# Performance work log

Hardware: AMD Instinct MI355X
Metric: run time of the kernel (lower is better)

## Reference

```python
import jax, jax.numpy as jnp
import numpy as np

B, L, ENC, EMB, H, V = 64, 33, 512, 256, 512, 32000


def setup_inputs() -> dict:
    key = jax.random.key(0)
    ks = jax.random.split(key, 16)
    x = jax.random.normal(ks[0], (B, ENC), dtype=jnp.float32)
    padded_target = jax.random.randint(ks[1], (B, L), 0, V)
    target_lengths = jax.random.randint(ks[2], (B,), 2, L + 1)
    target_lengths = target_lengths.at[0].set(L)  # pin max length -> static step count
    s = 0.05
    return {
        "x": x,
        "padded_target": padded_target,
        "target_lengths": target_lengths,
        "embed": jax.random.normal(ks[3], (V, EMB), dtype=jnp.float32) * s,
        "W_h0": jax.random.normal(ks[4], (H, ENC), dtype=jnp.float32) * s,
        "b_h0": jnp.zeros((H,), jnp.float32),
        "W_c0": jax.random.normal(ks[5], (H, ENC), dtype=jnp.float32) * s,
        "b_c0": jnp.zeros((H,), jnp.float32),
        "W_ih": jax.random.normal(ks[6], (4 * H, ENC + EMB), dtype=jnp.float32) * s,
        "W_hh": jax.random.normal(ks[7], (4 * H, H), dtype=jnp.float32) * s,
        "b_ih": jnp.zeros((4 * H,), jnp.float32),
        "b_hh": jnp.zeros((4 * H,), jnp.float32),
        "W_out": jax.random.normal(ks[8], (V, H), dtype=jnp.float32) * s,
        "b_out": jnp.zeros((V,), jnp.float32),
    }


def reference(x, padded_target, target_lengths, embed, W_h0, b_h0, W_c0, b_c0,
              W_ih, W_hh, b_ih, b_hh, W_out, b_out):
    # sort by length, descending (packed-sequence ordering)
    sorted_indices = jnp.argsort(-target_lengths)
    x = x[sorted_indices]                      # [B, ENC]
    tgt = padded_target[sorted_indices]        # [B, L]
    lens = target_lengths[sorted_indices] - 1  # decode steps per row
    emb = embed[tgt]                           # [B, L, EMB]

    h = x @ W_h0.T + b_h0                      # context-initialized state
    c = x @ W_c0.T + b_c0
    T = padded_target.shape[1] - 1             # static max steps (max len pinned to L)

    def step(carry, inp):
        h, c = carry
        e_t, t = inp
        active = (lens > t)[:, None]           # rows still decoding (prefix, sorted)
        g = jnp.concatenate([x, e_t], axis=1) @ W_ih.T + b_ih + h @ W_hh.T + b_hh
        i, f, gg, o = jnp.split(g, 4, axis=1)  # torch LSTMCell gate order i,f,g,o
        c_new = jax.nn.sigmoid(f) * c + jax.nn.sigmoid(i) * jnp.tanh(gg)
        h_new = jax.nn.sigmoid(o) * jnp.tanh(c_new)
        h = jnp.where(active, h_new, h)        # inactive rows keep frozen state
        c = jnp.where(active, c_new, c)
        pred = jnp.where(active, h_new @ W_out.T + b_out, 0.0)  # dropout p=0
        return (h, c), pred

    (_, _), preds = jax.lax.scan(
        step, (h, c), (jnp.transpose(emb[:, :T], (1, 0, 2)), jnp.arange(T)))
    prediction = jnp.transpose(preds, (1, 0, 2))  # [B, T, V]
    return prediction, sorted_indices
```

## Files before the change

### kernel.cpp

```cpp
#include <hip/hip_runtime.h>

typedef __attribute__((ext_vector_type(8))) short short8;
typedef __attribute__((ext_vector_type(8))) unsigned short ushort8;
typedef __attribute__((ext_vector_type(4))) float f32x4;

#define DEV __device__ __forceinline__

DEV unsigned short f2bf(float f) {
  unsigned int u = __float_as_uint(f);
  u += 0x7fffu + ((u >> 16) & 1u);
  return (unsigned short)(u >> 16);
}
DEV float sigm(float x) { return 1.f / (1.f + __expf(-x)); }
DEV float tanh_(float x) { return 1.f - 2.f / (1.f + __expf(2.f * x)); }

typedef __attribute__((address_space(1))) const void* as1cv;
typedef __attribute__((address_space(3))) void* as3v;
DEV void gll16(const void* g, void* l) {
  __builtin_amdgcn_global_load_lds((as1cv)g, (as3v)l, 16, 0, 0);
}

__global__ void __launch_bounds__(256) k_pre(const float* __restrict__ x,
    const int* __restrict__ ptar, const int* __restrict__ tlen,
    const float* __restrict__ W_h0, const float* __restrict__ W_c0,
    const float* __restrict__ W_ih, const float* __restrict__ W_hh,
    int* __restrict__ sidx, int* __restrict__ lens, int* __restrict__ base,
    int* __restrict__ inv, int* __restrict__ Pw, int* __restrict__ tok,
    unsigned short* __restrict__ xsb, float* __restrict__ tail,
    unsigned short* __restrict__ Wpro, unsigned short* __restrict__ Wihb2,
    unsigned short* __restrict__ Whb) {
  int bid = blockIdx.x, tid = threadIdx.x;
  if (bid > 0) {
    long long g = (long long)(bid - 1) * 2048 + tid * 8;
    const float* src;
    unsigned short* dst;
    if (g < 262144) {
      src = W_h0 + g; dst = Wpro + g;
    } else if (g < 524288) {
      long long l = g - 262144; src = W_c0 + l; dst = Wpro + 262144 + l;
    } else if (g < 1572864) {
      long long l = g - 524288;
      long long r = l >> 9, c = l & 511;
      src = W_ih + r * 768 + c; dst = Wpro + 524288 + l;
    } else if (g < 2097152) {
      long long l = g - 1572864;
      long long r = l >> 8, c = l & 255;
      src = W_ih + r * 768 + 512 + c; dst = Wihb2 + l;
    } else {
      long long l = g - 2097152; src = W_hh + l; dst = Whb + l;
    }
    float4 v0 = *(const float4*)src, v1 = *(const float4*)(src + 4);
    ushort8 o;
    o[0] = f2bf(v0.x); o[1] = f2bf(v0.y); o[2] = f2bf(v0.z); o[3] = f2bf(v0.w);
    o[4] = f2bf(v1.x); o[5] = f2bf(v1.y); o[6] = f2bf(v1.z); o[7] = f2bf(v1.w);
    *(ushort8*)dst = o;
    return;
  }
  __shared__ int ss[64], ls[64], bs[64];
  if (tid < 64) {
    int li = tlen[tid];
    int rank = 0;
    for (int j = 0; j < 64; ++j) {
      int lj = tlen[j];
      rank += (lj > li || (lj == li && j < tid)) ? 1 : 0;
    }
    ss[rank] = tid;
  }
  __syncthreads();
  if (tid < 64) {
    int src = ss[tid];
    sidx[tid] = src;
    int l = tlen[src] - 1;
    ls[tid] = l;
    lens[tid] = l;
    tail[tid] = (float)src;
  }
  __syncthreads();
  if (tid == 0) {
    int s = 0;
    for (int b = 0; b < 64; ++b) { bs[b] = s; base[b] = s; s += ls[b]; }
    Pw[0] = s;
  }
  __syncthreads();
  for (int idx = tid; idx < 2048; idx += 256) {
    int b = idx >> 5, t = idx & 31;
    if (t < ls[b]) inv[bs[b] + t] = idx;
  }
  for (int idx = tid; idx < 32 * 64; idx += 256) {
    int t = idx >> 6, b = idx & 63;
    tok[idx] = ptar[ss[b] * 33 + t];
  }
  for (int idx = tid; idx < 64 * 512; idx += 256) {
    int b = idx >> 9;
    xsb[idx] = f2bf(x[ss[b] * 512 + (idx & 511)]);
  }
}

__global__ void __launch_bounds__(256) k_mid(const unsigned short* __restrict__ xsb,
    const unsigned short* __restrict__ Wpro, const float* __restrict__ b_h0,
    const float* __restrict__ b_c0, const float* __restrict__ b_ih,
    const float* __restrict__ b_hh, unsigned short* __restrict__ h0b,
    float* __restrict__ c, float* __restrict__ gx,
    const int* __restrict__ tok, const float* __restrict__ embed,
    unsigned short* __restrict__ Eb) {
  int bid = blockIdx.x, tid = threadIdx.x;
  if (bid >= 48) {
    int gid = (bid - 48) * 256 + tid;
    int row = gid >> 5, c8 = (gid & 31) * 8;
    const float* src = embed + (size_t)tok[row] * 256 + c8;
    float4 v0 = *(const float4*)src, v1 = *(const float4*)(src + 4);
    ushort8 o;
    o[0] = f2bf(v0.x); o[1] = f2bf(v0.y); o[2] = f2bf(v0.z); o[3] = f2bf(v0.w);
    o[4] = f2bf(v1.x); o[5] = f2bf(v1.y); o[6] = f2bf(v1.z); o[7] = f2bf(v1.w);
    *(ushort8*)(Eb + (size_t)row * 256 + c8) = o;
    return;
  }
  int lane = tid & 63, w = tid >> 6;
  int n0 = bid * 64 + w * 16;
  int lr = lane & 15, lk = lane >> 4;
  f32x4 acc[4];
#pragma unroll
  for (int i = 0; i < 4; ++i) acc[i] = (f32x4){0.f, 0.f, 0.f, 0.f};
  const unsigned short* B = Wpro + (size_t)(n0 + lr) * 512 + lk * 8;
  const unsigned short* A = xsb + (size_t)lr * 512 + lk * 8;
#pragma unroll
  for (int ks = 0; ks < 16; ++ks) {
    short8 bfr = *(const short8*)(B + ks * 32);
#pragma unroll
    for (int mi = 0; mi < 4; ++mi) {
      short8 af = *(const short8*)(A + mi * 16 * 512 + ks * 32);
      acc[mi] = __builtin_amdgcn_mfma_f32_16x16x32_bf16(af, bfr, acc[mi], 0, 0, 0);
    }
  }
  int n = n0 + lr;
#pragma unroll
  for (int mi = 0; mi < 4; ++mi)
#pragma unroll
    for (int r = 0; r < 4; ++r) {
      int b = mi * 16 + lk * 4 + r;
      float v = acc[mi][r];
      if (n < 512) {
        h0b[b * 512 + n] = f2bf(v + b_h0[n]);
      } else if (n < 1024) {
        int u = n - 512;
        c[b * 512 + u] = v + b_c0[u];
      } else {
        int j = n - 1024;
        gx[(size_t)b * 2048 + j] = v + b_ih[j] + b_hh[j];
      }
    }
}

__global__ void __launch_bounds__(256) k_ga2(const unsigned short* __restrict__ Eb,
    const unsigned short* __restrict__ Wb2, const float* __restrict__ gx,
    float* __restrict__ GA) {
  __shared__ alignas(16) char ldsbuf[32768];
  char* ldsA = ldsbuf;
  char* ldsB = ldsbuf + 16384;
  int bid = blockIdx.x, tid = threadIdx.x;
  int mt = bid & 15, nt = bid >> 4;
  int m0 = mt * 128, n0 = nt * 128;
  int lane = tid & 63, w = tid >> 6;
  int wm = w >> 1, wn = w & 1;
  f32x4 acc[4][4];
#pragma unroll
  for (int a = 0; a < 4; ++a)
#pragma unroll
    for (int bq = 0; bq < 4; ++bq) acc[a][bq] = (f32x4){0.f, 0.f, 0.f, 0.f};
  const unsigned short* Arow = Eb + (size_t)m0 * 256;
  const unsigned short* Brow = Wb2 + (size_t)n0 * 256;
  for (int kt = 0; kt < 4; ++kt) {
    int k0 = kt * 64;
    if (kt) __syncthreads();
#pragma unroll
    for (int j = 0; j < 4; ++j) {
      int ci = j * 256 + w * 64 + lane;
      int r = ci >> 3;
      int clog = ((ci & 7) << 4) ^ ((r & 7) << 4);
      int ldst = (j * 256 + w * 64) * 16;
      gll16((const char*)(Arow + (size_t)r * 256 + k0) + clog, ldsA + ldst);
      gll16((const char*)(Brow + (size_t)r * 256 + k0) + clog, ldsB + ldst);
    }
    __syncthreads();
#pragma unroll
    for (int kk = 0; kk < 2; ++kk) {
      short8 af[4], bf[4];
      int cb = kk * 64 + (lane >> 4) * 16;
#pragma unroll
      for (int i = 0; i < 4; ++i) {
        int ar = wm * 64 + i * 16 + (lane & 15);
        af[i] = *(const short8*)(ldsA + ar * 128 + (cb ^ ((ar & 7) << 4)));
        int br = wn * 64 + i * 16 + (lane & 15);
        bf[i] = *(const short8*)(ldsB + br * 128 + (cb ^ ((br & 7) << 4)));
      }
#pragma unroll
      for (int mi = 0; mi < 4; ++mi)
#pragma unroll
        for (int ni = 0; ni < 4; ++ni)
          acc[mi][ni] = __builtin_amdgcn_mfma_f32_16x16x32_bf16(
              af[mi], bf[ni], acc[mi][ni], 0, 0, 0);
    }
  }
#pragma unroll
  for (int mi = 0; mi < 4; ++mi) {
    int mb = m0 + wm * 64 + mi * 16 + ((lane >> 4) << 2);
#pragma unroll
    for (int r = 0; r < 4; ++r) {
      int m = mb + r;
#pragma unroll
      for (int ni = 0; ni < 4; ++ni) {
        int j = n0 + wn * 64 + ni * 16 + (lane & 15);
        GA[(size_t)m * 2048 + j] = acc[mi][ni][r] + gx[(size_t)(m & 63) * 2048 + j];
      }
    }
  }
}

__global__ void __launch_bounds__(256) k_step4(
    const unsigned short* __restrict__ hin, unsigned short* __restrict__ hout,
    float* __restrict__ c, const float* __restrict__ GA,
    const unsigned short* __restrict__ Whb, const int* __restrict__ lens,
    const int* __restrict__ base, unsigned short* __restrict__ Hm,
    const float* __restrict__ W_out, unsigned short* __restrict__ Wob, int t) {
  int tid = threadIdx.x, bid = blockIdx.x;
  if (bid >= 128) {
    long long s0 = (long long)t * 512000 + (long long)(bid - 128) * 8000;
    long long s1 = s0 + 8000;
    for (long long i = s0 + tid * 8; i < s1; i += 2048) {
      float4 v0 = *(const float4*)(W_out + i);
      float4 v1 = *(const float4*)(W_out + i + 4);
      ushort8 o;
      o[0] = f2bf(v0.x); o[1] = f2bf(v0.y); o[2] = f2bf(v0.z); o[3] = f2bf(v0.w);
      o[4] = f2bf(v1.x); o[5] = f2bf(v1.y); o[6] = f2bf(v1.z); o[7] = f2bf(v1.w);
      *(ushort8*)(Wob + i) = o;
    }
    return;
  }
  int lane = tid & 63, w = tid >> 6;
  int lr = lane & 15, lk = lane >> 4;
  int mq = bid & 3, ug = bid >> 2;
  int r0 = mq * 16;
  int gate = lr >> 2, ul = lr & 3;
  int u = ug * 16 + w * 4 + ul;

  const float* gab = GA + ((size_t)t * 64 + r0) * 2048 + gate * 512 + u;
  float gv[4];
#pragma unroll
  for (int r = 0; r < 4; ++r) gv[r] = gab[(size_t)(lk * 4 + r) * 2048];

  const unsigned short* Bp = Whb + ((size_t)gate * 512 + u) * 512 + lk * 8;
  const unsigned short* Ap = hin + (size_t)(r0 + lr) * 512 + lk * 8;
  f32x4 acc = (f32x4){0.f, 0.f, 0.f, 0.f};
#pragma unroll
  for (int ks = 0; ks < 16; ++ks) {
    short8 a0 = *(const short8*)(Ap + ks * 32);
    short8 b0 = *(const short8*)(Bp + ks * 32);
    acc = __builtin_amdgcn_mfma_f32_16x16x32_bf16(a0, b0, acc, 0, 0, 0);
  }
#pragma unroll
  for (int r = 0; r < 4; ++r) {
    float v = acc[r] + gv[r];
    float av = (gate == 2) ? tanh_(v) : sigm(v);
    float x4 = __shfl_xor(av, 4);
    float x8 = __shfl_xor(av, 8);
    float x12 = __shfl_xor(av, 12);
    float vi = (gate == 0) ? av : (gate == 1) ? x4 : (gate == 2) ? x8 : x12;
    float vf = (gate == 1) ? av : (gate == 0) ? x4 : (gate == 3) ? x8 : x12;
    float vg = (gate == 2) ? av : (gate == 3) ? x4 : (gate == 0) ? x8 : x12;
    float vo = (gate == 3) ? av : (gate == 2) ? x4 : (gate == 1) ? x8 : x12;
    if (gate == 0) {
      int b = r0 + lk * 4 + r;
      float cold = c[b * 512 + u];
      float cn = vf * cold + vi * vg;
      float hn = vo * tanh_(cn);
      bool act = lens[b] > t;
      if (act) c[b * 512 + u] = cn;
      unsigned short hbv = f2bf(hn);
      hout[b * 512 + u] = act ? hbv : hin[b * 512 + u];
      if (act) Hm[((size_t)(base[b] + t)) * 512 + u] = hbv;
    }
  }
}

__global__ void __launch_bounds__(256) k_gemm(const unsigned short* __restrict__ Hm,
    const unsigned short* __restrict__ Wb, const float* __restrict__ b_out,
    const int* __restrict__ inv, const int* __restrict__ Pw,
    const int* __restrict__ lens, float* __restrict__ out) {
  int bid = blockIdx.x, tid = threadIdx.x;
  if (bid >= 4000) {
    int idx = bid - 4000;
    float4 z = {0.f, 0.f, 0.f, 0.f};
#pragma unroll
    for (int k = 0; k < 4; ++k) {
      int m = idx * 4 + k;
      int b = m >> 5, t = m & 31;
      if (lens[b] > t) continue;
      float* row = out + (size_t)m * 32000;
      for (int i = tid * 4; i < 32000; i += 1024) *(float4*)(row + i) = z;
    }
    return;
  }
  __shared__ alignas(16) char ldsbuf[32768];
  char* ldsA = ldsbuf;
  char* ldsB = ldsbuf + 16384;
  int P = Pw[0];
  int sb = (bid & 7) * 500 + (bid >> 3);
  int mt = sb & 15, nt = sb >> 4;
  int m0 = mt * 128, n0 = nt * 128;
  if (m0 >= P) return;
  int lane = tid & 63, w = tid >> 6;
  int wm = w >> 1, wn = w & 1;
  f32x4 acc[4][4];
#pragma unroll
  for (int a = 0; a < 4; ++a)
#pragma unroll
    for (int bq = 0; bq < 4; ++bq) acc[a][bq] = (f32x4){0.f, 0.f, 0.f, 0.f};
  const unsigned short* Arow = Hm + (size_t)m0 * 512;
  const unsigned short* Brow = Wb + (size_t)n0 * 512;
  for (int kt = 0; kt < 8; ++kt) {
    int k0 = kt * 64;
    if (kt) __syncthreads();
#pragma unroll
    for (int j = 0; j < 4; ++j) {
      int ci = j * 256 + w * 64 + lane;
      int r = ci >> 3;
      int clog = ((ci & 7) << 4) ^ ((r & 7) << 4);
      int ldst = (j * 256 + w * 64) * 16;
      gll16((const char*)(Arow + (size_t)r * 512 + k0) + clog, ldsA + ldst);
      gll16((const char*)(Brow + (size_t)r * 512 + k0) + clog, ldsB + ldst);
    }
    __syncthreads();
#pragma unroll
    for (int kk = 0; kk < 2; ++kk) {
      short8 af[4], bf[4];
      int cb = kk * 64 + (lane >> 4) * 16;
#pragma unroll
      for (int i = 0; i < 4; ++i) {
        int ar = wm * 64 + i * 16 + (lane & 15);
        af[i] = *(const short8*)(ldsA + ar * 128 + (cb ^ ((ar & 7) << 4)));
        int br = wn * 64 + i * 16 + (lane & 15);
        bf[i] = *(const short8*)(ldsB + br * 128 + (cb ^ ((br & 7) << 4)));
      }
#pragma unroll
      for (int mi = 0; mi < 4; ++mi)
#pragma unroll
        for (int ni = 0; ni < 4; ++ni)
          acc[mi][ni] = __builtin_amdgcn_mfma_f32_16x16x32_bf16(
              af[mi], bf[ni], acc[mi][ni], 0, 0, 0);
    }
  }
#pragma unroll
  for (int mi = 0; mi < 4; ++mi) {
    int pb = m0 + wm * 64 + mi * 16 + ((lane >> 4) << 2);
#pragma unroll
    for (int r = 0; r < 4; ++r) {
      int p = pb + r;
      if (p >= P) continue;
      size_t orow = (size_t)inv[p] * 32000;
#pragma unroll
      for (int ni = 0; ni < 4; ++ni) {
        int n = n0 + wn * 64 + ni * 16 + (lane & 15);
        out[orow + n] = acc[mi][ni][r] + b_out[n];
      }
    }
  }
}

extern "C" void kernel_launch(void* const* d_in, const int* in_sizes, int n_in,
                              void* d_out, int out_size, void* d_ws, size_t ws_size,
                              hipStream_t stream) {
  const float* x     = (const float*)d_in[0];
  const int*   ptar  = (const int*)d_in[1];
  const int*   tlen  = (const int*)d_in[2];
  const float* embed = (const float*)d_in[3];
  const float* W_h0  = (const float*)d_in[4];
  const float* b_h0  = (const float*)d_in[5];
  const float* W_c0  = (const float*)d_in[6];
  const float* b_c0  = (const float*)d_in[7];
  const float* W_ih  = (const float*)d_in[8];
  const float* W_hh  = (const float*)d_in[9];
  const float* b_ih  = (const float*)d_in[10];
  const float* b_hh  = (const float*)d_in[11];
  const float* W_out = (const float*)d_in[12];
  const float* b_out = (const float*)d_in[13];
  float* out = (float*)d_out;

  char* ws = (char*)d_ws;
  size_t off = 0;
  auto alloc = [&](size_t bytes) {
    void* p = ws + off;
    off += (bytes + 255) & ~(size_t)255;
    return p;
  };
  unsigned short* Wob = (unsigned short*)alloc(32000ull * 512 * 2);
  unsigned short* Hm  = (unsigned short*)alloc(2048ull * 512 * 2);
  unsigned short* h0b = (unsigned short*)alloc(64 * 512 * 2);
  unsigned short* h1b = (unsigned short*)alloc(64 * 512 * 2);
  float* cbuf = (float*)alloc(64 * 512 * 4);
  float* gx   = (float*)alloc(64 * 2048 * 4);
  int* sidx = (int*)alloc(64 * 4);
  int* lens = (int*)alloc(64 * 4);
  int* base = (int*)alloc(64 * 4);
  int* inv  = (int*)alloc(2048 * 4);
  int* Pw   = (int*)alloc(4);
  int* tok  = (int*)alloc(2048 * 4);

  float* GA = out;
  unsigned short* Wpro  = (unsigned short*)(out + 4194304);
  unsigned short* Wihb2 = (unsigned short*)(out + 4980736);
  unsigned short* Whb   = (unsigned short*)(out + 5242880);
  unsigned short* Eb    = (unsigned short*)(out + 5767168);
  unsigned short* xsb   = (unsigned short*)(out + 6029312);
  float* tail = out + 65536000;

  k_pre<<<1537, 256, 0, stream>>>(x, ptar, tlen, W_h0, W_c0, W_ih, W_hh,
                                  sidx, lens, base, inv, Pw, tok, xsb, tail,
                                  Wpro, Wihb2, Whb);
  k_mid<<<304, 256, 0, stream>>>(xsb, Wpro, b_h0, b_c0, b_ih, b_hh, h0b, cbuf,
                                 gx, tok, embed, Eb);
  k_ga2<<<256, 256, 0, stream>>>(Eb, Wihb2, gx, GA);

  unsigned short* hb[2] = {h0b, h1b};
  for (int t = 0; t < 32; ++t)
    k_step4<<<192, 256, 0, stream>>>(hb[t & 1], hb[(t + 1) & 1], cbuf, GA, Whb,
                                     lens, base, Hm, W_out, Wob, t);

  k_gemm<<<4512, 256, 0, stream>>>(Hm, Wob, b_out, inv, Pw, lens, out);
  (void)in_sizes; (void)n_in; (void)out_size; (void)ws_size;
}
```

Before: 394.4 us.

## Move W_out bf16 conversion into k_ga2 and load GEMM A operand directly

The fp32-to-bf16 conversion of W_out, previously spread across the 32 recurrent step launches as extra blocks, now runs as 500 extra blocks of the one-shot k_ga2 launch. This makes each step kernel smaller and possibly lowers per-step latency. In the output GEMM, the A operand (hidden states) is now read straight from global memory into registers instead of being staged through LDS, which halves the shared memory per block. The trade-off is uncoalesced, unswizzled global reads for A, which may rely on cache hits.

Result: slower. 450.7 us (+14.3%).

```diff
diff --git a/kernel.cpp b/kernel.cpp
--- a/kernel.cpp
+++ b/kernel.cpp
@@ -153,11 +153,26 @@
 
 __global__ void __launch_bounds__(256) k_ga2(const unsigned short* __restrict__ Eb,
     const unsigned short* __restrict__ Wb2, const float* __restrict__ gx,
-    float* __restrict__ GA) {
+    float* __restrict__ GA, const float* __restrict__ W_out,
+    unsigned short* __restrict__ Wob) {
+  int bid = blockIdx.x, tid = threadIdx.x;
+  if (bid >= 256) {
+    long long basei = (long long)(bid - 256) * 32768;
+#pragma unroll 4
+    for (int it = 0; it < 16; ++it) {
+      long long i = basei + (long long)it * 2048 + tid * 8;
+      float4 v0 = *(const float4*)(W_out + i);
+      float4 v1 = *(const float4*)(W_out + i + 4);
+      ushort8 o;
+      o[0] = f2bf(v0.x); o[1] = f2bf(v0.y); o[2] = f2bf(v0.z); o[3] = f2bf(v0.w);
+      o[4] = f2bf(v1.x); o[5] = f2bf(v1.y); o[6] = f2bf(v1.z); o[7] = f2bf(v1.w);
+      *(ushort8*)(Wob + i) = o;
+    }
+    return;
+  }
   __shared__ alignas(16) char ldsbuf[32768];
   char* ldsA = ldsbuf;
   char* ldsB = ldsbuf + 16384;
-  int bid = blockIdx.x, tid = threadIdx.x;
   int mt = bid & 15, nt = bid >> 4;
   int m0 = mt * 128, n0 = nt * 128;
   int lane = tid & 63, w = tid >> 6;
@@ -220,22 +235,8 @@
     const unsigned short* __restrict__ hin, unsigned short* __restrict__ hout,
     float* __restrict__ c, const float* __restrict__ GA,
     const unsigned short* __restrict__ Whb, const int* __restrict__ lens,
-    const int* __restrict__ base, unsigned short* __restrict__ Hm,
-    const float* __restrict__ W_out, unsigned short* __restrict__ Wob, int t) {
+    const int* __restrict__ base, unsigned short* __restrict__ Hm, int t) {
   int tid = threadIdx.x, bid = blockIdx.x;
-  if (bid >= 128) {
-    long long s0 = (long long)t * 512000 + (long long)(bid - 128) * 8000;
-    long long s1 = s0 + 8000;
-    for (long long i = s0 + tid * 8; i < s1; i += 2048) {
-      float4 v0 = *(const float4*)(W_out + i);
-      float4 v1 = *(const float4*)(W_out + i + 4);
-      ushort8 o;
-      o[0] = f2bf(v0.x); o[1] = f2bf(v0.y); o[2] = f2bf(v0.z); o[3] = f2bf(v0.w);
-      o[4] = f2bf(v1.x); o[5] = f2bf(v1.y); o[6] = f2bf(v1.z); o[7] = f2bf(v1.w);
-      *(ushort8*)(Wob + i) = o;
-    }
-    return;
-  }
   int lane = tid & 63, w = tid >> 6;
   int lr = lane & 15, lk = lane >> 4;
   int mq = bid & 3, ug = bid >> 2;
@@ -300,9 +301,7 @@
     }
     return;
   }
-  __shared__ alignas(16) char ldsbuf[32768];
-  char* ldsA = ldsbuf;
-  char* ldsB = ldsbuf + 16384;
+  __shared__ alignas(16) char ldsB[16384];
   int P = Pw[0];
   int sb = (bid & 7) * 500 + (bid >> 3);
   int mt = sb & 15, nt = sb >> 4;
@@ -315,7 +314,7 @@
   for (int a = 0; a < 4; ++a)
 #pragma unroll
     for (int bq = 0; bq < 4; ++bq) acc[a][bq] = (f32x4){0.f, 0.f, 0.f, 0.f};
-  const unsigned short* Arow = Hm + (size_t)m0 * 512;
+  const char* Ab = (const char*)(Hm + (size_t)m0 * 512);
   const unsigned short* Brow = Wb + (size_t)n0 * 512;
   for (int kt = 0; kt < 8; ++kt) {
     int k0 = kt * 64;
@@ -325,19 +324,25 @@
       int ci = j * 256 + w * 64 + lane;
       int r = ci >> 3;
       int clog = ((ci & 7) << 4) ^ ((r & 7) << 4);
-      int ldst = (j * 256 + w * 64) * 16;
-      gll16((const char*)(Arow + (size_t)r * 512 + k0) + clog, ldsA + ldst);
-      gll16((const char*)(Brow + (size_t)r * 512 + k0) + clog, ldsB + ldst);
-    }
-    __syncthreads();
-#pragma unroll
-    for (int kk = 0; kk < 2; ++kk) {
-      short8 af[4], bf[4];
-      int cb = kk * 64 + (lane >> 4) * 16;
+      gll16((const char*)(Brow + (size_t)r * 512 + k0) + clog,
+            ldsB + (j * 256 + w * 64) * 16);
+    }
+    short8 af2[2][4];
+#pragma unroll
+    for (int kk = 0; kk < 2; ++kk)
 #pragma unroll
       for (int i = 0; i < 4; ++i) {
         int ar = wm * 64 + i * 16 + (lane & 15);
-        af[i] = *(const short8*)(ldsA + ar * 128 + (cb ^ ((ar & 7) << 4)));
+        int cb = kk * 64 + (lane >> 4) * 16;
+        af2[kk][i] = *(const short8*)(Ab + (size_t)ar * 1024 + k0 * 2 + cb);
+      }
+    __syncthreads();
+#pragma unroll
+    for (int kk = 0; kk < 2; ++kk) {
+      short8 bf[4];
+      int cb = kk * 64 + (lane >> 4) * 16;
+#pragma unroll
+      for (int i = 0; i < 4; ++i) {
         int br = wn * 64 + i * 16 + (lane & 15);
         bf[i] = *(const short8*)(ldsB + br * 128 + (cb ^ ((br & 7) << 4)));
       }
@@ -346,7 +351,7 @@
 #pragma unroll
         for (int ni = 0; ni < 4; ++ni)
           acc[mi][ni] = __builtin_amdgcn_mfma_f32_16x16x32_bf16(
-              af[mi], bf[ni], acc[mi][ni], 0, 0, 0);
+              af2[kk][mi], bf[ni], acc[mi][ni], 0, 0, 0);
     }
   }
 #pragma unroll
@@ -418,12 +423,12 @@
                                   Wpro, Wihb2, Whb);
   k_mid<<<304, 256, 0, stream>>>(xsb, Wpro, b_h0, b_c0, b_ih, b_hh, h0b, cbuf,
                                  gx, tok, embed, Eb);
-  k_ga2<<<256, 256, 0, stream>>>(Eb, Wihb2, gx, GA);
+  k_ga2<<<756, 256, 0, stream>>>(Eb, Wihb2, gx, GA, W_out, Wob);
 
   unsigned short* hb[2] = {h0b, h1b};
   for (int t = 0; t < 32; ++t)
-    k_step4<<<192, 256, 0, stream>>>(hb[t & 1], hb[(t + 1) & 1], cbuf, GA, Whb,
-                                     lens, base, Hm, W_out, Wob, t);
+    k_step4<<<128, 256, 0, stream>>>(hb[t & 1], hb[(t + 1) & 1], cbuf, GA, Whb,
+                                     lens, base, Hm, t);
 
   k_gemm<<<4512, 256, 0, stream>>>(Hm, Wob, b_out, inv, Pw, lens, out);
   (void)in_sizes; (void)n_in; (void)out_size; (void)ws_size;
```

## Fuse 32 LSTM step launches into one persistent kernel with grid barrier

Applied to the files above, without the earlier changes.

Replaces the per-timestep launches of the recurrent step kernel with a single persistent kernel. Its 128 compute blocks loop over the timesteps and synchronise through atomic counters in global memory, which k_pre zeroes. Blocks whose row-group has finished decoding skip the step compute but still join each barrier. The W_out to bf16 conversion now runs in 128 extra blocks that stream through the whole weight at once instead of one slice per step. This removes launch overhead, but it depends on all 256 blocks being co-resident and adds spin-wait latency on every step.

After: 653.8 us. +65.8%, slower.

```diff
diff --git a/kernel.cpp b/kernel.cpp
--- a/kernel.cpp
+++ b/kernel.cpp
@@ -28,7 +28,7 @@
     int* __restrict__ inv, int* __restrict__ Pw, int* __restrict__ tok,
     unsigned short* __restrict__ xsb, float* __restrict__ tail,
     unsigned short* __restrict__ Wpro, unsigned short* __restrict__ Wihb2,
-    unsigned short* __restrict__ Whb) {
+    unsigned short* __restrict__ Whb, int* __restrict__ bar) {
   int bid = blockIdx.x, tid = threadIdx.x;
   if (bid > 0) {
     long long g = (long long)(bid - 1) * 2048 + tid * 8;
@@ -57,6 +57,7 @@
     return;
   }
   __shared__ int ss[64], ls[64], bs[64];
+  if (tid < 32) bar[tid] = 0;
   if (tid < 64) {
     int li = tlen[tid];
     int rank = 0;
@@ -216,17 +217,17 @@
   }
 }
 
-__global__ void __launch_bounds__(256) k_step4(
-    const unsigned short* __restrict__ hin, unsigned short* __restrict__ hout,
+__global__ void __launch_bounds__(256) k_steps_p(
+    unsigned short* __restrict__ h0, unsigned short* __restrict__ h1,
     float* __restrict__ c, const float* __restrict__ GA,
     const unsigned short* __restrict__ Whb, const int* __restrict__ lens,
     const int* __restrict__ base, unsigned short* __restrict__ Hm,
-    const float* __restrict__ W_out, unsigned short* __restrict__ Wob, int t) {
+    int* __restrict__ bar,
+    const float* __restrict__ W_out, unsigned short* __restrict__ Wob) {
   int tid = threadIdx.x, bid = blockIdx.x;
   if (bid >= 128) {
-    long long s0 = (long long)t * 512000 + (long long)(bid - 128) * 8000;
-    long long s1 = s0 + 8000;
-    for (long long i = s0 + tid * 8; i < s1; i += 2048) {
+    for (long long i = ((long long)(bid - 128) * 256 + tid) * 8; i < 16384000LL;
+         i += 128LL * 256 * 8) {
       float4 v0 = *(const float4*)(W_out + i);
       float4 v1 = *(const float4*)(W_out + i + 4);
       ushort8 o;
@@ -242,43 +243,61 @@
   int r0 = mq * 16;
   int gate = lr >> 2, ul = lr & 3;
   int u = ug * 16 + w * 4 + ul;
-
-  const float* gab = GA + ((size_t)t * 64 + r0) * 2048 + gate * 512 + u;
-  float gv[4];
-#pragma unroll
-  for (int r = 0; r < 4; ++r) gv[r] = gab[(size_t)(lk * 4 + r) * 2048];
-
-  const unsigned short* Bp = Whb + ((size_t)gate * 512 + u) * 512 + lk * 8;
-  const unsigned short* Ap = hin + (size_t)(r0 + lr) * 512 + lk * 8;
-  f32x4 acc = (f32x4){0.f, 0.f, 0.f, 0.f};
-#pragma unroll
-  for (int ks = 0; ks < 16; ++ks) {
-    short8 a0 = *(const short8*)(Ap + ks * 32);
-    short8 b0 = *(const short8*)(Bp + ks * 32);
-    acc = __builtin_amdgcn_mfma_f32_16x16x32_bf16(a0, b0, acc, 0, 0, 0);
-  }
-#pragma unroll
-  for (int r = 0; r < 4; ++r) {
-    float v = acc[r] + gv[r];
-    float av = (gate == 2) ? tanh_(v) : sigm(v);
-    float x4 = __shfl_xor(av, 4);
-    float x8 = __shfl_xor(av, 8);
-    float x12 = __shfl_xor(av, 12);
-    float vi = (gate == 0) ? av : (gate == 1) ? x4 : (gate == 2) ? x8 : x12;
-    float vf = (gate == 1) ? av : (gate == 0) ? x4 : (gate == 3) ? x8 : x12;
-    float vg = (gate == 2) ? av : (gate == 3) ? x4 : (gate == 0) ? x8 : x12;
-    float vo = (gate == 3) ? av : (gate == 2) ? x4 : (gate == 1) ? x8 : x12;
-    if (gate == 0) {
-      int b = r0 + lk * 4 + r;
-      float cold = c[b * 512 + u];
-      float cn = vf * cold + vi * vg;
-      float hn = vo * tanh_(cn);
-      bool act = lens[b] > t;
-      if (act) c[b * 512 + u] = cn;
-      unsigned short hbv = f2bf(hn);
-      hout[b * 512 + u] = act ? hbv : hin[b * 512 + u];
-      if (act) Hm[((size_t)(base[b] + t)) * 512 + u] = hbv;
-    }
+  int lim = lens[r0];
+
+  for (int t = 0; t < 32; ++t) {
+    const unsigned short* hin = (t & 1) ? h1 : h0;
+    unsigned short* hout = (t & 1) ? h0 : h1;
+    if (t <= lim) {
+      const float* gab = GA + ((size_t)t * 64 + r0) * 2048 + gate * 512 + u;
+      float gv[4];
+#pragma unroll
+      for (int r = 0; r < 4; ++r) gv[r] = gab[(size_t)(lk * 4 + r) * 2048];
+      const unsigned short* Bp = Whb + ((size_t)gate * 512 + u) * 512 + lk * 8;
+      const unsigned short* Ap = hin + (size_t)(r0 + lr) * 512 + lk * 8;
+      f32x4 acc = (f32x4){0.f, 0.f, 0.f, 0.f};
+#pragma unroll
+      for (int ks = 0; ks < 16; ++ks) {
+        short8 a0 = *(const short8*)(Ap + ks * 32);
+        short8 b0 = *(const short8*)(Bp + ks * 32);
+        acc = __builtin_amdgcn_mfma_f32_16x16x32_bf16(a0, b0, acc, 0, 0, 0);
+      }
+#pragma unroll
+      for (int r = 0; r < 4; ++r) {
+        float v = acc[r] + gv[r];
+        float av = (gate == 2) ? tanh_(v) : sigm(v);
+        float x4 = __shfl_xor(av, 4);
+        float x8 = __shfl_xor(av, 8);
+        float x12 = __shfl_xor(av, 12);
+        float vi = (gate == 0) ? av : (gate == 1) ? x4 : (gate == 2) ? x8 : x12;
+        float vf = (gate == 1) ? av : (gate == 0) ? x4 : (gate == 3) ? x8 : x12;
+        float vg = (gate == 2) ? av : (gate == 3) ? x4 : (gate == 0) ? x8 : x12;
+        float vo = (gate == 3) ? av : (gate == 2) ? x4 : (gate == 1) ? x8 : x12;
+        if (gate == 0) {
+          int b = r0 + lk * 4 + r;
+          float cold = c[b * 512 + u];
+          float cn = vf * cold + vi * vg;
+          float hn = vo * tanh_(cn);
+          bool act = lens[b] > t;
+          if (act) c[b * 512 + u] = cn;
+          unsigned short hbv = f2bf(hn);
+          hout[b * 512 + u] = act ? hbv : hin[b * 512 + u];
+          if (act) Hm[((size_t)(base[b] + t)) * 512 + u] = hbv;
+        }
+      }
+    }
+    if (t == 31) break;
+    __syncthreads();
+    if (tid == 0) {
+      __threadfence();
+      __hip_atomic_fetch_add(&bar[t], 1, __ATOMIC_RELAXED,
+                             __HIP_MEMORY_SCOPE_AGENT);
+      while (__hip_atomic_load(&bar[t], __ATOMIC_RELAXED,
+                               __HIP_MEMORY_SCOPE_AGENT) < 128)
+        __builtin_amdgcn_s_sleep(2);
+      __threadfence();
+    }
+    __syncthreads();
   }
 }
 
@@ -404,6 +423,7 @@
   int* inv  = (int*)alloc(2048 * 4);
   int* Pw   = (int*)alloc(4);
   int* tok  = (int*)alloc(2048 * 4);
+  int* bar  = (int*)alloc(32 * 4);
 
   float* GA = out;
   unsigned short* Wpro  = (unsigned short*)(out + 4194304);
@@ -415,16 +435,12 @@
 
   k_pre<<<1537, 256, 0, stream>>>(x, ptar, tlen, W_h0, W_c0, W_ih, W_hh,
                                   sidx, lens, base, inv, Pw, tok, xsb, tail,
-                                  Wpro, Wihb2, Whb);
+                                  Wpro, Wihb2, Whb, bar);
   k_mid<<<304, 256, 0, stream>>>(xsb, Wpro, b_h0, b_c0, b_ih, b_hh, h0b, cbuf,
                                  gx, tok, embed, Eb);
   k_ga2<<<256, 256, 0, stream>>>(Eb, Wihb2, gx, GA);
-
-  unsigned short* hb[2] = {h0b, h1b};
-  for (int t = 0; t < 32; ++t)
-    k_step4<<<192, 256, 0, stream>>>(hb[t & 1], hb[(t + 1) & 1], cbuf, GA, Whb,
-                                     lens, base, Hm, W_out, Wob, t);
-
+  k_steps_p<<<256, 256, 0, stream>>>(h0b, h1b, cbuf, GA, Whb, lens, base, Hm,
+                                     bar, W_out, Wob);
   k_gemm<<<4512, 256, 0, stream>>>(Hm, Wob, b_out, inv, Pw, lens, out);
   (void)in_sizes; (void)n_in; (void)out_size; (void)ws_size;
 }
```
